# Performance work log

Hardware: AMD Instinct MI355X
Metric: run time of the kernel (lower is better)

## Reference

```python
import jax, jax.numpy as jnp
import numpy as np

B, S, D = 4, 1024, 1024      # batch, seq, dim
H = 1024                     # moe_inter_dim
E = 16                       # n_routed_experts
K = 2                        # n_activated_experts (top-k)
N_IN = 2                     # experts that consume x instead of embeddings
NSH = 2                      # n_shared_experts


def setup_inputs() -> dict:
    key = jax.random.key(0)
    ks = jax.random.split(key, 10)
    s = 0.02
    return {
        "embeddings": jax.random.normal(ks[0], (B, S, D), dtype=jnp.float32),
        "x": jax.random.normal(ks[1], (B * S, D), dtype=jnp.float32),
        "gate_w": jax.random.normal(ks[2], (E, D), dtype=jnp.float32) * s,
        "W1": jax.random.normal(ks[3], (E, D, H), dtype=jnp.float32) * s,
        "B1": jnp.zeros((E, H), dtype=jnp.float32),
        "W2": jax.random.normal(ks[4], (E, H, D), dtype=jnp.float32) * s,
        "B2": jnp.zeros((E, D), dtype=jnp.float32),
        "W3": jax.random.normal(ks[5], (E, D, H), dtype=jnp.float32) * s,
        "B3": jnp.zeros((E, H), dtype=jnp.float32),
        "sW1": jax.random.normal(ks[6], (D, NSH * H), dtype=jnp.float32) * s,
        "sB1": jnp.zeros((NSH * H,), dtype=jnp.float32),
        "sW2": jax.random.normal(ks[7], (NSH * H, D), dtype=jnp.float32) * s,
        "sB2": jnp.zeros((D,), dtype=jnp.float32),
    }


def _experts(inp, W1, B1, W2, B2, W3, B3):
    # SwiGLU expert applied for a stack of experts: inp [T,D], W* [e,...]
    h = jax.nn.silu(jnp.einsum('td,edh->eth', inp, W1) + B1[:, None, :]) \
        * (jnp.einsum('td,edh->eth', inp, W3) + B3[:, None, :])
    return jnp.einsum('eth,ehd->etd', h, W2) + B2[:, None, :]


def reference(embeddings, x, gate_w, W1, B1, W2, B2, W3, B3, sW1, sB1, sW2, sB2):
    shape = embeddings.shape
    emb = embeddings.reshape(-1, D)                       # [T, D]
    # Gate: softmax scores in fp32; n_groups==1, bias is None -> no group masking
    scores = jax.nn.softmax((emb @ gate_w.T).astype(jnp.float32), axis=-1)  # [T, E]
    top_w, top_i = jax.lax.top_k(scores, K)               # weights == gathered original_scores
    weights = top_w.astype(emb.dtype)                     # route_scale = 1.0
    # Combine coefficient per (token, expert): sum of routing weights of slots hitting e
    c = jnp.einsum('tk,tke->te', weights,
                   jax.nn.one_hot(top_i, E, dtype=weights.dtype))  # [T, E]
    # First N_IN experts consume x; the rest consume the embeddings
    out_in = _experts(x, W1[:N_IN], B1[:N_IN], W2[:N_IN], B2[:N_IN], W3[:N_IN], B3[:N_IN])
    out_emb = _experts(emb, W1[N_IN:], B1[N_IN:], W2[N_IN:], B2[N_IN:], W3[N_IN:], B3[N_IN:])
    y = jnp.einsum('te,etd->td', c, jnp.concatenate([out_in, out_emb], axis=0))
    # Shared experts (applied to every token)
    z = jax.nn.silu(emb @ sW1 + sB1) @ sW2 + sB2
    return (y + z).reshape(shape)
```

## Files before the change

### kernel.cpp

```cpp
#include <hip/hip_runtime.h>

#define T_TOK 4096
#define DIM   1024
#define HID   1024
#define NEXP  16
#define HSH   2048
#define NIN   2
#define MT_MAX 80

typedef __attribute__((ext_vector_type(8))) short bf8_t;
typedef __attribute__((ext_vector_type(4))) float f4_t;

__device__ __forceinline__ ushort f2b(float f) {
  unsigned u = __float_as_uint(f);
  u = (u + 0x7FFFu + ((u >> 16) & 1u)) >> 16;
  return (ushort)u;
}

__device__ __forceinline__ int tp_off(int r, int c) {
  return r * 64 + ((((c >> 3) ^ (r & 7)) << 3) | (c & 7));
}
__device__ __forceinline__ size_t tp_idx(int row, int col, int KT) {
  return ((size_t)((row >> 7) * KT + (col >> 6)) << 13) + tp_off(row & 127, col & 63);
}

__device__ __forceinline__ void gl_lds16(const ushort* g, ushort* l) {
  __builtin_amdgcn_global_load_lds(
      (const __attribute__((address_space(1))) void*)g,
      (__attribute__((address_space(3))) void*)l, 16, 0, 0);
}

template<bool DUAL>
__device__ __forceinline__ void mfma_tp(
    const ushort* __restrict__ aT, const ushort* __restrict__ b1T,
    const ushort* __restrict__ b3T, int nkt,
    ushort* As, ushort* Bs1, ushort* Bs3,
    f4_t acc1[4][4], f4_t acc3[4][4], int tid)
{
  const int lane = tid & 63, w = tid >> 6;
  const int wm = w & 1, wn = w >> 1;
  const int quad = lane >> 4, lr = lane & 15;
  const int soff = w << 11;
  const int l8 = lane * 8;

  for (int kt = 0; kt < nkt; kt++) {
    const size_t tb = (size_t)kt << 13;
    const ushort* ga = aT + tb + soff + l8;
    const ushort* gb = b1T + tb + soff + l8;
    #pragma unroll
    for (int d = 0; d < 4; d++) {
      gl_lds16(ga + (d << 9), As  + soff + (d << 9));
      gl_lds16(gb + (d << 9), Bs1 + soff + (d << 9));
    }
    if (DUAL) {
      const ushort* gc = b3T + tb + soff + l8;
      #pragma unroll
      for (int d = 0; d < 4; d++)
        gl_lds16(gc + (d << 9), Bs3 + soff + (d << 9));
    }
    __syncthreads();
    #pragma unroll
    for (int half = 0; half < 2; half++) {
      const int ch = (half << 2) + quad;
      bf8_t af[4];
      #pragma unroll
      for (int mi = 0; mi < 4; mi++) {
        const int r = wm * 64 + mi * 16 + lr;
        af[mi] = *(const bf8_t*)&As[r * 64 + ((ch ^ (r & 7)) << 3)];
      }
      #pragma unroll
      for (int ni = 0; ni < 4; ni++) {
        const int n = wn * 64 + ni * 16 + lr;
        bf8_t b1 = *(const bf8_t*)&Bs1[n * 64 + ((ch ^ (n & 7)) << 3)];
        #pragma unroll
        for (int mi = 0; mi < 4; mi++)
          acc1[mi][ni] = __builtin_amdgcn_mfma_f32_16x16x32_bf16(af[mi], b1, acc1[mi][ni], 0, 0, 0);
        if (DUAL) {
          bf8_t b3 = *(const bf8_t*)&Bs3[n * 64 + ((ch ^ (n & 7)) << 3)];
          #pragma unroll
          for (int mi = 0; mi < 4; mi++)
            acc3[mi][ni] = __builtin_amdgcn_mfma_f32_16x16x32_bf16(af[mi], b3, acc3[mi][ni], 0, 0, 0);
        }
      }
    }
    __syncthreads();
  }
}

__device__ __forceinline__ void tr_band(const float* __restrict__ src,
                                        ushort* __restrict__ dst,
                                        int R, int C, int band, int tid,
                                        ushort* ts)
{
  const int KT = R >> 6;
  const int k0g = band * 64;
  const int nchunk = C >> 8;
  for (int c = 0; c < nchunk; c++) {
    #pragma unroll
    for (int i = 0; i < 16; i++) {
      const int idx = i * 256 + tid;
      const int r = idx >> 6, c4 = idx & 63;
      const float4 v = *(const float4*)(src + (size_t)(k0g + r) * C + c * 256 + c4 * 4);
      ushort4 u;
      u.x = f2b(v.x); u.y = f2b(v.y); u.z = f2b(v.z); u.w = f2b(v.w);
      *(ushort4*)&ts[r * 264 + c4 * 4] = u;
    }
    __syncthreads();
    #pragma unroll
    for (int s = 0; s < 2; s++) {
      const int m = s * 256 + tid;
      const int ng = m & 63, kc = m >> 6;
      ushort vv[32];
      #pragma unroll
      for (int j = 0; j < 8; j++)
        *(ushort4*)&vv[j * 4] = *(const ushort4*)&ts[(kc * 8 + j) * 264 + ng * 4];
      #pragma unroll
      for (int i = 0; i < 4; i++) {
        ushort o[8];
        #pragma unroll
        for (int j = 0; j < 8; j++) o[j] = vv[j * 4 + i];
        const int n = c * 256 + ng * 4 + i;
        *(uint4*)&dst[tp_idx(n, k0g + kc * 8, KT)] = *(uint4*)o;
      }
    }
    __syncthreads();
  }
}

#define PREP_BLOCKS 5936
__global__ void prep(const float* __restrict__ emb, const float* __restrict__ x_,
                     const float* __restrict__ gw,
                     const float* __restrict__ W1, const float* __restrict__ W3,
                     const float* __restrict__ W2,
                     const float* __restrict__ sW1, const float* __restrict__ sW2,
                     ushort* __restrict__ embf, ushort* __restrict__ xf,
                     ushort* __restrict__ etp,
                     ushort* __restrict__ w1tp, ushort* __restrict__ w3tp,
                     ushort* __restrict__ w2tp,
                     ushort* __restrict__ sw1tp, ushort* __restrict__ sw2tp,
                     int* __restrict__ eA, int* __restrict__ eB,
                     float* __restrict__ wA, float* __restrict__ wB)
{
  __shared__ ushort smem[64 * 264];
  const int b = blockIdx.x;
  const int t = threadIdx.x;

  if (b < 4096) {
    float* se = (float*)smem;
    float* sc = (float*)smem + DIM;
    const int tok = b;
    ((float4*)se)[t] = ((const float4*)(emb + (size_t)tok * DIM))[t];
    __syncthreads();
    const int e = t >> 4, l = t & 15;
    const float* g = gw + e * DIM + l * 4;
    const float* s = se + l * 4;
    float p = 0.f;
    #pragma unroll
    for (int j = 0; j < 16; j++) {
      const float4 gv = *(const float4*)(g + j * 64);
      const float4 sv = *(const float4*)(s + j * 64);
      p += gv.x * sv.x + gv.y * sv.y + gv.z * sv.z + gv.w * sv.w;
    }
    p += __shfl_xor(p, 1); p += __shfl_xor(p, 2);
    p += __shfl_xor(p, 4); p += __shfl_xor(p, 8);
    if (l == 0) sc[e] = p;
    __syncthreads();
    if (t == 0) {
      float m = sc[0];
      #pragma unroll
      for (int j = 1; j < NEXP; j++) m = fmaxf(m, sc[j]);
      float pr[NEXP]; float sum = 0.f;
      #pragma unroll
      for (int j = 0; j < NEXP; j++) { pr[j] = __expf(sc[j] - m); sum += pr[j]; }
      const float inv = 1.0f / sum;
      int i0 = 0; float b0 = pr[0];
      #pragma unroll
      for (int j = 1; j < NEXP; j++) if (pr[j] > b0) { b0 = pr[j]; i0 = j; }
      int i1 = -1; float b1 = -1.f;
      #pragma unroll
      for (int j = 0; j < NEXP; j++) if (j != i0 && pr[j] > b1) { b1 = pr[j]; i1 = j; }
      eA[tok] = i0; wA[tok] = b0 * inv;
      eB[tok] = i1; wB[tok] = b1 * inv;
    }
  } else if (b < 5120) {
    const int NC = (T_TOK * DIM) / 8;
    const int c0 = (b - 4096) * 256 + t;
    for (int c = c0; c < 2 * NC; c += 1024 * 256) {
      const bool isE = c < NC;
      const int g = (isE ? c : c - NC) << 3;
      const float* src = isE ? emb : x_;
      const float4 v0 = *(const float4*)(src + g);
      const float4 v1 = *(const float4*)(src + g + 4);
      ushort tt[8];
      tt[0] = f2b(v0.x); tt[1] = f2b(v0.y); tt[2] = f2b(v0.z); tt[3] = f2b(v0.w);
      tt[4] = f2b(v1.x); tt[5] = f2b(v1.y); tt[6] = f2b(v1.z); tt[7] = f2b(v1.w);
      ushort* flat = isE ? embf : xf;
      *(uint4*)(flat + g) = *(uint4*)tt;
      if (isE) {
        const int row = g >> 10, col = g & 1023;
        *(uint4*)&etp[tp_idx(row, col, 16)] = *(uint4*)tt;
      }
    }
  } else if (b < 5888) {
    const int r = b - 5120;
    const int z = r >> 4, band = r & 15;
    const float* src = (z < 16) ? W1 : (z < 32) ? W3 : W2;
    ushort* dst = (z < 16) ? w1tp : (z < 32) ? w3tp : w2tp;
    tr_band(src + ((size_t)(z & 15) << 20), dst + ((size_t)(z & 15) << 20),
            1024, 1024, band, t, smem);
  } else if (b < 5904) {
    tr_band(sW1, sw1tp, DIM, HSH, b - 5888, t, smem);
  } else {
    tr_band(sW2, sw2tp, HSH, DIM, b - 5904, t, smem);
  }
}

__global__ void build_lists(const int* __restrict__ eA, const int* __restrict__ eB,
                            const float* __restrict__ wA, const float* __restrict__ wB,
                            int* __restrict__ cnt, int* __restrict__ list,
                            float* __restrict__ wl)
{
  const int e = blockIdx.x;
  __shared__ int wsum[4];
  __shared__ int sbase;
  const int tid = threadIdx.x;
  const int lane = tid & 63, wv = tid >> 6;
  if (tid == 0) sbase = 0;
  __syncthreads();
  for (int r = 0; r < 16; r++) {
    const int tk = r * 256 + tid;
    const int a = eA[tk], bb = eB[tk];
    const bool m = (a == e) || (bb == e);
    const float w = (a == e) ? wA[tk] : wB[tk];
    const unsigned long long bal = __ballot(m);
    const int pw = __popcll(bal & ((1ULL << lane) - 1ULL));
    if (lane == 63) wsum[wv] = pw + (m ? 1 : 0);
    __syncthreads();
    int base = sbase;
    for (int k = 0; k < wv; k++) base += wsum[k];
    if (m) {
      const int pos = base + pw;
      list[e * T_TOK + pos] = tk;
      wl[e * T_TOK + pos] = w;
    }
    __syncthreads();
    if (tid == 0) sbase += wsum[0] + wsum[1] + wsum[2] + wsum[3];
    __syncthreads();
  }
  if (tid == 0) cnt[e] = sbase;
}

__global__ void scan_offs(const int* __restrict__ cnt, int* __restrict__ offp,
                          int* __restrict__ tbl)
{
  if (blockIdx.x == 0 && threadIdx.x == 0) {
    int a = 0, nm = 0;
    for (int e = 0; e < NEXP; e++) {
      offp[e] = a;
      const int c = (cnt[e] + 127) & ~127;
      for (int r = 0; r < c; r += 128) { tbl[2 * nm] = e; tbl[2 * nm + 1] = a + r; nm++; }
      a += c;
    }
    offp[NEXP] = a;
    offp[NEXP + 1] = nm;
  }
}

__global__ void gather_a(const ushort* __restrict__ embf, const ushort* __restrict__ xf,
                         const int* __restrict__ cnt, const int* __restrict__ offp,
                         const int* __restrict__ tbl, const int* __restrict__ list,
                         ushort* __restrict__ ag)
{
  const int mt = blockIdx.x >> 3;
  if (mt >= offp[NEXP + 1]) return;
  const int sl = blockIdx.x & 7;
  const int e = tbl[2 * mt], row0 = tbl[2 * mt + 1];
  const int ce = cnt[e];
  const int s0 = row0 - offp[e];
  const ushort* src = (e < NIN) ? xf : embf;
  const int tid = threadIdx.x;
  #pragma unroll
  for (int rep = 0; rep < 8; rep++) {
    const int lin = rep * 256 + tid;
    const int r = lin >> 4, c8 = (sl * 128) + ((lin & 15) << 3);
    const int s = s0 + r;
    uint4 v = make_uint4(0u, 0u, 0u, 0u);
    if (s < ce) {
      const int tok = list[e * T_TOK + s];
      v = *(const uint4*)&src[(size_t)tok * DIM + c8];
    }
    *(uint4*)&ag[tp_idx(row0 + r, c8, 16)] = v;
  }
}

__launch_bounds__(256, 3)
__global__ void stage1(const ushort* __restrict__ ag, const ushort* __restrict__ etp,
                       const ushort* __restrict__ w1tp, const ushort* __restrict__ w3tp,
                       const ushort* __restrict__ sw1tp,
                       const float* __restrict__ B1, const float* __restrict__ B3,
                       const float* __restrict__ sB1,
                       const int* __restrict__ offp, const int* __restrict__ tbl,
                       ushort* __restrict__ h_tp, ushort* __restrict__ hs_tp)
{
  __shared__ ushort As[8192], Bs1[8192], Bs3[8192];
  const int tid = threadIdx.x;
  const int lane = tid & 63, w = tid >> 6;
  const int wm = w & 1, wn = w >> 1;
  const int quad = lane >> 4, lr = lane & 15;
  const int b = blockIdx.x;

  f4_t acc1[4][4], acc3[4][4];
  const f4_t fz = {0.f, 0.f, 0.f, 0.f};
  #pragma unroll
  for (int i = 0; i < 4; i++)
    #pragma unroll
    for (int j = 0; j < 4; j++) { acc1[i][j] = fz; acc3[i][j] = fz; }

  if (b < 512) {
    const int m0 = (b >> 4) << 7;
    const int n0 = (b & 15) << 7;
    const ushort* aT = etp + ((size_t)((m0 >> 7) * 16) << 13);
    const ushort* bT = sw1tp + ((size_t)((n0 >> 7) * 16) << 13);
    mfma_tp<false>(aT, bT, nullptr, 16, As, Bs1, Bs3, acc1, acc3, tid);
    #pragma unroll
    for (int mi = 0; mi < 4; mi++) {
      #pragma unroll
      for (int r = 0; r < 4; r++) {
        const int row = m0 + wm * 64 + mi * 16 + quad * 4 + r;
        #pragma unroll
        for (int ni = 0; ni < 4; ni++) {
          const int col = n0 + wn * 64 + ni * 16 + lr;
          const float v = acc1[mi][ni][r] + sB1[col];
          const float sg = 1.0f / (1.0f + __expf(-v));
          hs_tp[tp_idx(row, col, 32)] = f2b(v * sg);
        }
      }
    }
  } else {
    const int t = b - 512;
    const int mt = t >> 3;
    if (mt >= offp[NEXP + 1]) return;
    const int n0 = (t & 7) << 7;
    const int e = tbl[2 * mt], row0 = tbl[2 * mt + 1];
    const ushort* aT  = ag + ((size_t)((row0 >> 7) * 16) << 13);
    const ushort* b1T = w1tp + ((size_t)e << 20) + ((size_t)((n0 >> 7) * 16) << 13);
    const ushort* b3T = w3tp + ((size_t)e << 20) + ((size_t)((n0 >> 7) * 16) << 13);
    mfma_tp<true>(aT, b1T, b3T, 16, As, Bs1, Bs3, acc1, acc3, tid);
    #pragma unroll
    for (int mi = 0; mi < 4; mi++) {
      #pragma unroll
      for (int r = 0; r < 4; r++) {
        const int grow = row0 + wm * 64 + mi * 16 + quad * 4 + r;
        #pragma unroll
        for (int ni = 0; ni < 4; ni++) {
          const int col = n0 + wn * 64 + ni * 16 + lr;
          const float v1 = acc1[mi][ni][r] + B1[e * HID + col];
          const float v3 = acc3[mi][ni][r] + B3[e * HID + col];
          const float sg = 1.0f / (1.0f + __expf(-v1));
          h_tp[tp_idx(grow, col, 16)] = f2b(v1 * sg * v3);
        }
      }
    }
  }
}

__launch_bounds__(256, 4)
__global__ void stage2(const ushort* __restrict__ h_tp, const ushort* __restrict__ hs_tp,
                       const ushort* __restrict__ w2tp, const ushort* __restrict__ sw2tp,
                       const float* __restrict__ B2, const float* __restrict__ sB2,
                       const int* __restrict__ cnt, const int* __restrict__ offp,
                       const int* __restrict__ tbl, const int* __restrict__ list,
                       const float* __restrict__ wl, float* __restrict__ y)
{
  __shared__ ushort As[8192], Bs[8192];
  const int tid = threadIdx.x;
  const int lane = tid & 63, w = tid >> 6;
  const int wm = w & 1, wn = w >> 1;
  const int quad = lane >> 4, lr = lane & 15;
  const int b = blockIdx.x;

  f4_t acc[4][4];
  const f4_t fz = {0.f, 0.f, 0.f, 0.f};
  #pragma unroll
  for (int i = 0; i < 4; i++)
    #pragma unroll
    for (int j = 0; j < 4; j++) acc[i][j] = fz;

  if (b < 256) {
    const int m0 = (b >> 3) << 7;
    const int n0 = (b & 7) << 7;
    const ushort* aT = hs_tp + ((size_t)((m0 >> 7) * 32) << 13);
    const ushort* bT = sw2tp + ((size_t)((n0 >> 7) * 32) << 13);
    mfma_tp<false>(aT, bT, nullptr, 32, As, Bs, Bs, acc, acc, tid);
    #pragma unroll
    for (int mi = 0; mi < 4; mi++) {
      #pragma unroll
      for (int r = 0; r < 4; r++) {
        const int row = m0 + wm * 64 + mi * 16 + quad * 4 + r;
        float* yr = y + (size_t)row * DIM;
        #pragma unroll
        for (int ni = 0; ni < 4; ni++) {
          const int col = n0 + wn * 64 + ni * 16 + lr;
          atomicAdd(&yr[col], acc[mi][ni][r] + sB2[col]);
        }
      }
    }
  } else {
    const int t = b - 256;
    const int mt = t >> 3;
    if (mt >= offp[NEXP + 1]) return;
    const int n0 = (t & 7) << 7;
    const int e = tbl[2 * mt], row0 = tbl[2 * mt + 1];
    const int ce = cnt[e];
    const int s0 = row0 - offp[e];
    const ushort* aT = h_tp + ((size_t)((row0 >> 7) * 16) << 13);
    const ushort* bT = w2tp + ((size_t)e << 20) + ((size_t)((n0 >> 7) * 16) << 13);
    mfma_tp<false>(aT, bT, nullptr, 16, As, Bs, Bs, acc, acc, tid);
    #pragma unroll
    for (int mi = 0; mi < 4; mi++) {
      #pragma unroll
      for (int r = 0; r < 4; r++) {
        const int rowl = s0 + wm * 64 + mi * 16 + quad * 4 + r;
        if (rowl < ce) {
          const int tok = list[e * T_TOK + rowl];
          const float wgt = wl[e * T_TOK + rowl];
          float* yr = y + (size_t)tok * DIM;
          #pragma unroll
          for (int ni = 0; ni < 4; ni++) {
            const int col = n0 + wn * 64 + ni * 16 + lr;
            atomicAdd(&yr[col], wgt * (acc[mi][ni][r] + B2[e * DIM + col]));
          }
        }
      }
    }
  }
}

extern "C" void kernel_launch(void* const* d_in, const int* in_sizes, int n_in,
                              void* d_out, int out_size, void* d_ws, size_t ws_size,
                              hipStream_t stream)
{
  const float* emb = (const float*)d_in[0];
  const float* x   = (const float*)d_in[1];
  const float* gw  = (const float*)d_in[2];
  const float* W1  = (const float*)d_in[3];
  const float* B1  = (const float*)d_in[4];
  const float* W2  = (const float*)d_in[5];
  const float* B2  = (const float*)d_in[6];
  const float* W3  = (const float*)d_in[7];
  const float* B3  = (const float*)d_in[8];
  const float* sW1 = (const float*)d_in[9];
  const float* sB1 = (const float*)d_in[10];
  const float* sW2 = (const float*)d_in[11];
  const float* sB2 = (const float*)d_in[12];
  float* y = (float*)d_out;

  char* ws = (char*)d_ws;
  const size_t MB = 1024ULL * 1024ULL;
  ushort* embf  = (ushort*)(ws + 0);
  ushort* xf    = (ushort*)(ws + 8 * MB);
  ushort* etp   = (ushort*)(ws + 16 * MB);
  ushort* w1tp  = (ushort*)(ws + 24 * MB);
  ushort* w3tp  = (ushort*)(ws + 56 * MB);
  ushort* w2tp  = (ushort*)(ws + 88 * MB);
  ushort* sw1tp = (ushort*)(ws + 120 * MB);
  ushort* sw2tp = (ushort*)(ws + 124 * MB);
  ushort* ag    = (ushort*)(ws + 128 * MB);
  ushort* h_tp  = (ushort*)(ws + 148 * MB);
  ushort* hs_tp = (ushort*)(ws + 168 * MB);
  int*   cnt    = (int*)(ws + 184 * MB);
  int*   offp   = cnt + 16;
  int*   tbl    = offp + 18;
  int*   list   = (int*)(ws + 184 * MB + 1024);
  float* wl     = (float*)(ws + 184 * MB + 1024 + 262144);
  int*   eA     = (int*)(ws + 185 * MB);
  int*   eB     = eA + T_TOK;
  float* wA     = (float*)(eB + T_TOK);
  float* wB     = wA + T_TOK;

  hipMemsetAsync(y, 0, (size_t)T_TOK * DIM * sizeof(float), stream);
  prep<<<PREP_BLOCKS, 256, 0, stream>>>(emb, x, gw, W1, W3, W2, sW1, sW2,
                                        embf, xf, etp, w1tp, w3tp, w2tp,
                                        sw1tp, sw2tp, eA, eB, wA, wB);
  build_lists<<<NEXP, 256, 0, stream>>>(eA, eB, wA, wB, cnt, list, wl);
  scan_offs<<<1, 64, 0, stream>>>(cnt, offp, tbl);
  gather_a<<<MT_MAX * 8, 256, 0, stream>>>(embf, xf, cnt, offp, tbl, list, ag);
  stage1<<<512 + MT_MAX * 8, 256, 0, stream>>>(ag, etp, w1tp, w3tp, sw1tp,
                                               B1, B3, sB1, offp, tbl, h_tp, hs_tp);
  stage2<<<256 + MT_MAX * 8, 256, 0, stream>>>(h_tp, hs_tp, w2tp, sw2tp, B2, sB2,
                                               cnt, offp, tbl, list, wl, y);
}
```

Before: 556.9 us.

## Restructure prep kernel: finer transpose chunks, warp-level gating, drop flat bf16 copies

Weight transposes now run one 256-column chunk per block instead of looping over a whole band, which exposes more parallel blocks and puts them first in the grid. Gating moves to one wavefront per token, with top-2 selection done by shuffles and ballots instead of a single thread, so fewer blocks handle routing. The flat bf16 copies of emb and x are no longer written. x is stored in the tiled layout instead, and gather_a reads from the tiled buffers, which cuts prep write traffic. Launch bounds are added and the cast loop stride is adjusted to fit the new block count.

```diff
diff --git a/kernel.cpp b/kernel.cpp
--- a/kernel.cpp
+++ b/kernel.cpp
@@ -87,105 +87,112 @@
   }
 }
 
-__device__ __forceinline__ void tr_band(const float* __restrict__ src,
-                                        ushort* __restrict__ dst,
-                                        int R, int C, int band, int tid,
-                                        ushort* ts)
+__device__ __forceinline__ void tr_chunk(const float* __restrict__ src,
+                                         ushort* __restrict__ dst,
+                                         int R, int C, int band, int c, int tid,
+                                         ushort* ts)
 {
   const int KT = R >> 6;
-  const int k0g = band * 64;
-  const int nchunk = C >> 8;
-  for (int c = 0; c < nchunk; c++) {
-    #pragma unroll
-    for (int i = 0; i < 16; i++) {
-      const int idx = i * 256 + tid;
-      const int r = idx >> 6, c4 = idx & 63;
-      const float4 v = *(const float4*)(src + (size_t)(k0g + r) * C + c * 256 + c4 * 4);
-      ushort4 u;
-      u.x = f2b(v.x); u.y = f2b(v.y); u.z = f2b(v.z); u.w = f2b(v.w);
-      *(ushort4*)&ts[r * 264 + c4 * 4] = u;
-    }
-    __syncthreads();
-    #pragma unroll
-    for (int s = 0; s < 2; s++) {
-      const int m = s * 256 + tid;
-      const int ng = m & 63, kc = m >> 6;
-      ushort vv[32];
-      #pragma unroll
-      for (int j = 0; j < 8; j++)
-        *(ushort4*)&vv[j * 4] = *(const ushort4*)&ts[(kc * 8 + j) * 264 + ng * 4];
-      #pragma unroll
-      for (int i = 0; i < 4; i++) {
-        ushort o[8];
-        #pragma unroll
-        for (int j = 0; j < 8; j++) o[j] = vv[j * 4 + i];
-        const int n = c * 256 + ng * 4 + i;
-        *(uint4*)&dst[tp_idx(n, k0g + kc * 8, KT)] = *(uint4*)o;
-      }
-    }
-    __syncthreads();
-  }
-}
-
-#define PREP_BLOCKS 5936
+  const int k0 = band * 64;
+  #pragma unroll
+  for (int i = 0; i < 16; i++) {
+    const int idx = i * 256 + tid;
+    const int r = idx >> 6, c4 = idx & 63;
+    const float4 v = *(const float4*)(src + (size_t)(k0 + r) * C + c * 256 + c4 * 4);
+    ushort4 u;
+    u.x = f2b(v.x); u.y = f2b(v.y); u.z = f2b(v.z); u.w = f2b(v.w);
+    *(ushort4*)&ts[r * 264 + c4 * 4] = u;
+  }
+  __syncthreads();
+  #pragma unroll
+  for (int s = 0; s < 2; s++) {
+    const int m = s * 256 + tid;
+    const int ng = m & 63, kc = m >> 6;
+    ushort vv[32];
+    #pragma unroll
+    for (int j = 0; j < 8; j++)
+      *(ushort4*)&vv[j * 4] = *(const ushort4*)&ts[(kc * 8 + j) * 264 + ng * 4];
+    #pragma unroll
+    for (int i = 0; i < 4; i++) {
+      ushort o[8];
+      #pragma unroll
+      for (int j = 0; j < 8; j++) o[j] = vv[j * 4 + i];
+      const int n = c * 256 + ng * 4 + i;
+      *(uint4*)&dst[tp_idx(n, k0 + kc * 8, KT)] = *(uint4*)o;
+    }
+  }
+}
+
+#define PREP_BLOCKS 4864
+__launch_bounds__(256, 4)
 __global__ void prep(const float* __restrict__ emb, const float* __restrict__ x_,
                      const float* __restrict__ gw,
                      const float* __restrict__ W1, const float* __restrict__ W3,
                      const float* __restrict__ W2,
                      const float* __restrict__ sW1, const float* __restrict__ sW2,
-                     ushort* __restrict__ embf, ushort* __restrict__ xf,
-                     ushort* __restrict__ etp,
+                     ushort* __restrict__ etp, ushort* __restrict__ xtp,
                      ushort* __restrict__ w1tp, ushort* __restrict__ w3tp,
                      ushort* __restrict__ w2tp,
                      ushort* __restrict__ sw1tp, ushort* __restrict__ sw2tp,
                      int* __restrict__ eA, int* __restrict__ eB,
                      float* __restrict__ wA, float* __restrict__ wB)
 {
-  __shared__ ushort smem[64 * 264];
+  __shared__ ushort ts[64 * 264];
   const int b = blockIdx.x;
   const int t = threadIdx.x;
 
-  if (b < 4096) {
-    float* se = (float*)smem;
-    float* sc = (float*)smem + DIM;
-    const int tok = b;
-    ((float4*)se)[t] = ((const float4*)(emb + (size_t)tok * DIM))[t];
-    __syncthreads();
-    const int e = t >> 4, l = t & 15;
-    const float* g = gw + e * DIM + l * 4;
-    const float* s = se + l * 4;
+  if (b < 3328) {
+    const float* src; ushort* dst; int R, C, band, chunk;
+    if (b < 3072) {
+      const int z = b >> 6, rem = b & 63;
+      band = rem >> 2; chunk = rem & 3;
+      const int e = z & 15;
+      src = ((z < 16) ? W1 : (z < 32) ? W3 : W2) + ((size_t)e << 20);
+      dst = ((z < 16) ? w1tp : (z < 32) ? w3tp : w2tp) + ((size_t)e << 20);
+      R = 1024; C = 1024;
+    } else if (b < 3200) {
+      const int i = b - 3072; band = i >> 3; chunk = i & 7;
+      src = sW1; dst = sw1tp; R = 1024; C = 2048;
+    } else {
+      const int i = b - 3200; band = i >> 2; chunk = i & 3;
+      src = sW2; dst = sw2tp; R = 2048; C = 1024;
+    }
+    tr_chunk(src, dst, R, C, band, chunk, t, ts);
+  } else if (b < 4352) {
+    const int w = t >> 6, lane = t & 63;
+    const int tok = (b - 3328) * 4 + w;
+    const int e = lane & 15, q = lane >> 4;
+    const float* er = emb + (size_t)tok * DIM + q * 256;
+    const float* gr = gw + (size_t)e * DIM + q * 256;
     float p = 0.f;
-    #pragma unroll
-    for (int j = 0; j < 16; j++) {
-      const float4 gv = *(const float4*)(g + j * 64);
-      const float4 sv = *(const float4*)(s + j * 64);
-      p += gv.x * sv.x + gv.y * sv.y + gv.z * sv.z + gv.w * sv.w;
-    }
-    p += __shfl_xor(p, 1); p += __shfl_xor(p, 2);
-    p += __shfl_xor(p, 4); p += __shfl_xor(p, 8);
-    if (l == 0) sc[e] = p;
-    __syncthreads();
-    if (t == 0) {
-      float m = sc[0];
-      #pragma unroll
-      for (int j = 1; j < NEXP; j++) m = fmaxf(m, sc[j]);
-      float pr[NEXP]; float sum = 0.f;
-      #pragma unroll
-      for (int j = 0; j < NEXP; j++) { pr[j] = __expf(sc[j] - m); sum += pr[j]; }
+    #pragma unroll 8
+    for (int j = 0; j < 64; j++) {
+      const float4 a = *(const float4*)(er + j * 4);
+      const float4 g = *(const float4*)(gr + j * 4);
+      p += a.x * g.x + a.y * g.y + a.z * g.z + a.w * g.w;
+    }
+    p += __shfl_xor(p, 16); p += __shfl_xor(p, 32);
+    float m1 = p;
+    m1 = fmaxf(m1, __shfl_xor(m1, 1)); m1 = fmaxf(m1, __shfl_xor(m1, 2));
+    m1 = fmaxf(m1, __shfl_xor(m1, 4)); m1 = fmaxf(m1, __shfl_xor(m1, 8));
+    float sum = __expf(p - m1);
+    sum += __shfl_xor(sum, 1); sum += __shfl_xor(sum, 2);
+    sum += __shfl_xor(sum, 4); sum += __shfl_xor(sum, 8);
+    const int i0 = __ffsll(__ballot(p == m1) & 0xFFFFull) - 1;
+    const float p2 = (e == i0) ? -3.402823466e38f : p;
+    float m2 = p2;
+    m2 = fmaxf(m2, __shfl_xor(m2, 1)); m2 = fmaxf(m2, __shfl_xor(m2, 2));
+    m2 = fmaxf(m2, __shfl_xor(m2, 4)); m2 = fmaxf(m2, __shfl_xor(m2, 8));
+    const int i1 = __ffsll(__ballot(p2 == m2) & 0xFFFFull) - 1;
+    if (lane == 0) {
       const float inv = 1.0f / sum;
-      int i0 = 0; float b0 = pr[0];
-      #pragma unroll
-      for (int j = 1; j < NEXP; j++) if (pr[j] > b0) { b0 = pr[j]; i0 = j; }
-      int i1 = -1; float b1 = -1.f;
-      #pragma unroll
-      for (int j = 0; j < NEXP; j++) if (j != i0 && pr[j] > b1) { b1 = pr[j]; i1 = j; }
-      eA[tok] = i0; wA[tok] = b0 * inv;
-      eB[tok] = i1; wB[tok] = b1 * inv;
-    }
-  } else if (b < 5120) {
+      eA[tok] = i0; wA[tok] = inv;
+      eB[tok] = i1; wB[tok] = __expf(m2 - m1) * inv;
+    }
+  } else {
     const int NC = (T_TOK * DIM) / 8;
-    const int c0 = (b - 4096) * 256 + t;
-    for (int c = c0; c < 2 * NC; c += 1024 * 256) {
+    const int c0 = (b - 4352) * 256 + t;
+    for (int c = c0; c < 2 * NC; c += 512 * 256) {
       const bool isE = c < NC;
       const int g = (isE ? c : c - NC) << 3;
       const float* src = isE ? emb : x_;
@@ -194,24 +201,10 @@
       ushort tt[8];
       tt[0] = f2b(v0.x); tt[1] = f2b(v0.y); tt[2] = f2b(v0.z); tt[3] = f2b(v0.w);
       tt[4] = f2b(v1.x); tt[5] = f2b(v1.y); tt[6] = f2b(v1.z); tt[7] = f2b(v1.w);
-      ushort* flat = isE ? embf : xf;
-      *(uint4*)(flat + g) = *(uint4*)tt;
-      if (isE) {
-        const int row = g >> 10, col = g & 1023;
-        *(uint4*)&etp[tp_idx(row, col, 16)] = *(uint4*)tt;
-      }
-    }
-  } else if (b < 5888) {
-    const int r = b - 5120;
-    const int z = r >> 4, band = r & 15;
-    const float* src = (z < 16) ? W1 : (z < 32) ? W3 : W2;
-    ushort* dst = (z < 16) ? w1tp : (z < 32) ? w3tp : w2tp;
-    tr_band(src + ((size_t)(z & 15) << 20), dst + ((size_t)(z & 15) << 20),
-            1024, 1024, band, t, smem);
-  } else if (b < 5904) {
-    tr_band(sW1, sw1tp, DIM, HSH, b - 5888, t, smem);
-  } else {
-    tr_band(sW2, sw2tp, HSH, DIM, b - 5904, t, smem);
+      const int row = g >> 10, col = g & 1023;
+      ushort* dst = isE ? etp : xtp;
+      *(uint4*)&dst[tp_idx(row, col, 16)] = *(uint4*)tt;
+    }
   }
 }
 
@@ -266,7 +259,7 @@
   }
 }
 
-__global__ void gather_a(const ushort* __restrict__ embf, const ushort* __restrict__ xf,
+__global__ void gather_a(const ushort* __restrict__ etp, const ushort* __restrict__ xtp,
                          const int* __restrict__ cnt, const int* __restrict__ offp,
                          const int* __restrict__ tbl, const int* __restrict__ list,
                          ushort* __restrict__ ag)
@@ -277,7 +270,7 @@
   const int e = tbl[2 * mt], row0 = tbl[2 * mt + 1];
   const int ce = cnt[e];
   const int s0 = row0 - offp[e];
-  const ushort* src = (e < NIN) ? xf : embf;
+  const ushort* src = (e < NIN) ? xtp : etp;
   const int tid = threadIdx.x;
   #pragma unroll
   for (int rep = 0; rep < 8; rep++) {
@@ -287,7 +280,7 @@
     uint4 v = make_uint4(0u, 0u, 0u, 0u);
     if (s < ce) {
       const int tok = list[e * T_TOK + s];
-      v = *(const uint4*)&src[(size_t)tok * DIM + c8];
+      v = *(const uint4*)&src[tp_idx(tok, c8, 16)];
     }
     *(uint4*)&ag[tp_idx(row0 + r, c8, 16)] = v;
   }
@@ -457,8 +450,7 @@
 
   char* ws = (char*)d_ws;
   const size_t MB = 1024ULL * 1024ULL;
-  ushort* embf  = (ushort*)(ws + 0);
-  ushort* xf    = (ushort*)(ws + 8 * MB);
+  ushort* xtp   = (ushort*)(ws + 0);
   ushort* etp   = (ushort*)(ws + 16 * MB);
   ushort* w1tp  = (ushort*)(ws + 24 * MB);
   ushort* w3tp  = (ushort*)(ws + 56 * MB);
@@ -480,11 +472,11 @@
 
   hipMemsetAsync(y, 0, (size_t)T_TOK * DIM * sizeof(float), stream);
   prep<<<PREP_BLOCKS, 256, 0, stream>>>(emb, x, gw, W1, W3, W2, sW1, sW2,
-                                        embf, xf, etp, w1tp, w3tp, w2tp,
+                                        etp, xtp, w1tp, w3tp, w2tp,
                                         sw1tp, sw2tp, eA, eB, wA, wB);
   build_lists<<<NEXP, 256, 0, stream>>>(eA, eB, wA, wB, cnt, list, wl);
   scan_offs<<<1, 64, 0, stream>>>(cnt, offp, tbl);
-  gather_a<<<MT_MAX * 8, 256, 0, stream>>>(embf, xf, cnt, offp, tbl, list, ag);
+  gather_a<<<MT_MAX * 8, 256, 0, stream>>>(etp, xtp, cnt, offp, tbl, list, ag);
   stage1<<<512 + MT_MAX * 8, 256, 0, stream>>>(ag, etp, w1tp, w3tp, sw1tp,
                                                B1, B3, sB1, offp, tbl, h_tp, hs_tp);
   stage2<<<256 + MT_MAX * 8, 256, 0, stream>>>(h_tp, hs_tp, w2tp, sw2tp, B2, sB2,
```

Result: faster. 507.3 us (-8.9%).
